# Kernel tuning notes

Measured on AMD Instinct MI355X. Metric: run time of the kernel, lower is better.

Reference implementation:

```python
import jax, jax.numpy as jnp
import numpy as np

N = 8192
F_IN = 256
F_OUT = 64
ALPHA = 0.2  # LeakyReLU negative slope
EDGE_P = 0.004  # ~33 avg degree


def setup_inputs() -> dict:
    key = jax.random.key(0)
    k1, k2, k3, k4 = jax.random.split(key, 4)
    h = jax.random.normal(k1, (N, F_IN), dtype=jnp.float32)
    # xavier-ish scale for params
    W = jax.random.normal(k2, (F_IN, F_OUT), dtype=jnp.float32) * np.float32(np.sqrt(2.0 / (F_IN + F_OUT)))
    a = jax.random.normal(k3, (2 * F_OUT, 1), dtype=jnp.float32) * np.float32(np.sqrt(2.0 / (2 * F_OUT + 1)))
    adj = (jax.random.uniform(k4, (N, N)) < EDGE_P).astype(jnp.float32)
    return {"h": h, "adj": adj, "W": W, "a": a}


def reference(h, adj, W, a):
    f_out = W.shape[1]
    Wh = h @ W  # [N, F_OUT]
    # NOTE: original uses a[out_features:] for the source (row) term
    wh1 = Wh @ a[f_out:, :]  # [N, 1]
    wh2 = Wh @ a[:f_out, :]  # [N, 1]
    # e[u, i] = wh1[u] + wh2[i] only where adj nonzero; zero elsewhere (NO -inf mask,
    # faithful to the original: softmax sees zeros at non-edges)
    e = jnp.where(adj != 0, wh1 + wh2.T, jnp.float32(0.0))  # [N, N]
    e = jnp.where(e >= 0, e, ALPHA * e)  # LeakyReLU
    attention = jax.nn.softmax(e, axis=1)  # [N, N]
    # dropout p=0.0 -> identity
    h_prime = attention @ Wh  # [N, F_OUT]
    return jax.nn.elu(h_prime)  # concat=True
```

## Files before the change

### kernel.cpp

```cpp
#include <hip/hip_runtime.h>
#include <hip/hip_bf16.h>
#include <math.h>

#define N     8192
#define F_IN  256
#define F_OUT 64
#define ALPHA 0.2f

__global__ __launch_bounds__(256) void gat_wh_kernel(
    const float* __restrict__ h,
    const float* __restrict__ W,
    const float* __restrict__ a,
    float* __restrict__ Wh,
    float* __restrict__ wh1,
    float* __restrict__ wh2,
    float* __restrict__ colpart)
{
    __shared__ float s_h[4][F_IN];
    __shared__ float s_cp[256];

    const int tid = threadIdx.x;
    const int wv  = tid >> 6;
    const int ln  = tid & 63;
    const int u   = blockIdx.x * 4 + wv;

    const float4* hrow = (const float4*)(h + (size_t)u * F_IN);
    ((float4*)s_h[wv])[ln] = hrow[ln];
    __syncthreads();

    float acc = 0.f;
    const float4* sh4 = (const float4*)s_h[wv];
#pragma unroll 8
    for (int k4 = 0; k4 < F_IN / 4; ++k4) {
        float4 hv = sh4[k4];
        int k = k4 * 4;
        acc += hv.x * W[(k + 0) * F_OUT + ln];
        acc += hv.y * W[(k + 1) * F_OUT + ln];
        acc += hv.z * W[(k + 2) * F_OUT + ln];
        acc += hv.w * W[(k + 3) * F_OUT + ln];
    }

    Wh[(size_t)u * F_OUT + ln] = acc;

    float p1 = acc * a[F_OUT + ln];
    float p2 = acc * a[ln];
#pragma unroll
    for (int off = 32; off > 0; off >>= 1) {
        p1 += __shfl_down(p1, off);
        p2 += __shfl_down(p2, off);
    }
    if (ln == 0) {
        wh1[u] = p1;
        wh2[u] = p2;
    }

    s_cp[tid] = acc;
    __syncthreads();
    if (tid < 64) {
        colpart[(size_t)blockIdx.x * 64 + tid] =
            s_cp[tid] + s_cp[tid + 64] + s_cp[tid + 128] + s_cp[tid + 192];
    }
}

__global__ __launch_bounds__(256) void gat_colsum_kernel(
    const float* __restrict__ colpart,
    float* __restrict__ colsum)
{
    __shared__ float r[256];
    const int f = blockIdx.x;
    const int tid = threadIdx.x;
    float s = 0.f;
    for (int b = tid; b < 2048; b += 256) s += colpart[(size_t)b * 64 + f];
    r[tid] = s;
    __syncthreads();
    if (tid < 128) r[tid] += r[tid + 128];
    __syncthreads();
    if (tid < 64) {
        float x = r[tid] + r[tid + 64];
#pragma unroll
        for (int off = 32; off > 0; off >>= 1) x += __shfl_down(x, off);
        if (tid == 0) colsum[f] = x;
    }
}

#define CHUNK  2048
#define PASSES (N / CHUNK)

__global__ __launch_bounds__(256) void gat_main_kernel(
    const float* __restrict__ adj,
    const float* __restrict__ Wh,
    const float* __restrict__ wh1,
    const float* __restrict__ wh2,
    const float* __restrict__ colsum,
    float* __restrict__ out)
{
    __shared__ int   s_idx[CHUNK];
    __shared__ float s_w[CHUNK];
    __shared__ float s_red[256];
    __shared__ int   s_cnt;

    const int tid = threadIdx.x;
    const int u   = blockIdx.x;
    const int f   = tid & 63;
    const int g   = tid >> 6;

    const float wh1u = wh1[u];
    const float* __restrict__ arow = adj + (size_t)u * N;

    float acc  = 0.f;
    float sumw = 0.f;

    for (int p = 0; p < PASSES; ++p) {
        if (tid == 0) s_cnt = 0;
        __syncthreads();

        const int base = p * CHUNK + tid * 8;
        float4 v0 = *(const float4*)(arow + base);
        float4 v1 = *(const float4*)(arow + base + 4);
        float vals[8] = {v0.x, v0.y, v0.z, v0.w, v1.x, v1.y, v1.z, v1.w};
#pragma unroll
        for (int j = 0; j < 8; ++j) {
            if (vals[j] != 0.f) {
                int col = base + j;
                float e = wh1u + wh2[col];
                e = (e >= 0.f) ? e : ALPHA * e;
                float w = expm1f(e);
                sumw += w;
                int pos = atomicAdd(&s_cnt, 1);
                s_idx[pos] = col;
                s_w[pos]   = w;
            }
        }
        __syncthreads();
        const int nE = s_cnt;
        __syncthreads();

        for (int e = g; e < nE; e += 4) {
            acc += s_w[e] * Wh[(size_t)s_idx[e] * F_OUT + f];
        }
    }

    s_red[tid] = sumw;
    __syncthreads();
    if (tid < 128) s_red[tid] += s_red[tid + 128];
    __syncthreads();
    if (tid < 64) {
        float x = s_red[tid] + s_red[tid + 64];
#pragma unroll
        for (int off = 32; off > 0; off >>= 1) x += __shfl_down(x, off);
        if (tid == 0) s_red[0] = x;
    }
    __syncthreads();
    const float denom = s_red[0] + (float)N;
    __syncthreads();

    s_red[tid] = acc;
    __syncthreads();
    if (tid < 64) {
        float tot = s_red[tid] + s_red[tid + 64] + s_red[tid + 128] + s_red[tid + 192];
        float val = (tot + colsum[tid]) / denom;
        out[(size_t)u * F_OUT + tid] = (val > 0.f) ? val : expm1f(val);
    }
}

extern "C" void kernel_launch(void* const* d_in, const int* in_sizes, int n_in,
                              void* d_out, int out_size, void* d_ws, size_t ws_size,
                              hipStream_t stream) {
    const float* h   = (const float*)d_in[0];
    const float* adj = (const float*)d_in[1];
    const float* W   = (const float*)d_in[2];
    const float* a   = (const float*)d_in[3];
    float* out = (float*)d_out;

    float* ws      = (float*)d_ws;
    float* Wh      = ws;
    float* wh1     = Wh + (size_t)N * F_OUT;
    float* wh2     = wh1 + N;
    float* colpart = wh2 + N;
    float* colsum  = colpart + 2048 * 64;

    gat_wh_kernel<<<N / 4, 256, 0, stream>>>(h, W, a, Wh, wh1, wh2, colpart);
    gat_colsum_kernel<<<64, 256, 0, stream>>>(colpart, colsum);
    gat_main_kernel<<<N, 256, 0, stream>>>(adj, Wh, wh1, wh2, colsum, out);
}
```

Baseline: 393.5 us.

## Assign one wavefront per row and compact edges with ballot instead of shared atomics

The main kernel now gives each 64-lane wavefront one adjacency row, four rows per block, in place of one 256-thread block per row. Each wavefront scans the row with vector loads, finds nonzero edges with a ballot mask, and all lanes walk that mask together to accumulate the weighted Wh features. This removes the shared-memory atomic compaction, the block barriers and the cross-wave reductions. In exchange, each wave handles all edges of its row serially, and the adj loads have a different coalescing pattern.

```diff
diff --git a/kernel.cpp b/kernel.cpp
--- a/kernel.cpp
+++ b/kernel.cpp
@@ -83,9 +83,6 @@
     }
 }
 
-#define CHUNK  2048
-#define PASSES (N / CHUNK)
-
 __global__ __launch_bounds__(256) void gat_main_kernel(
     const float* __restrict__ adj,
     const float* __restrict__ Wh,
@@ -94,15 +91,10 @@
     const float* __restrict__ colsum,
     float* __restrict__ out)
 {
-    __shared__ int   s_idx[CHUNK];
-    __shared__ float s_w[CHUNK];
-    __shared__ float s_red[256];
-    __shared__ int   s_cnt;
-
-    const int tid = threadIdx.x;
-    const int u   = blockIdx.x;
-    const int f   = tid & 63;
-    const int g   = tid >> 6;
+    const int tid  = threadIdx.x;
+    const int lane = tid & 63;
+    const int wv   = tid >> 6;
+    const int u    = blockIdx.x * 4 + wv;
 
     const float wh1u = wh1[u];
     const float* __restrict__ arow = adj + (size_t)u * N;
@@ -110,57 +102,30 @@
     float acc  = 0.f;
     float sumw = 0.f;
 
-    for (int p = 0; p < PASSES; ++p) {
-        if (tid == 0) s_cnt = 0;
-        __syncthreads();
-
-        const int base = p * CHUNK + tid * 8;
-        float4 v0 = *(const float4*)(arow + base);
-        float4 v1 = *(const float4*)(arow + base + 4);
+    for (int it = 0; it < 16; ++it) {
+        const int cbase = it * 512;
+        const float4* p = (const float4*)(arow + cbase + lane * 8);
+        float4 v0 = p[0];
+        float4 v1 = p[1];
         float vals[8] = {v0.x, v0.y, v0.z, v0.w, v1.x, v1.y, v1.z, v1.w};
 #pragma unroll
         for (int j = 0; j < 8; ++j) {
-            if (vals[j] != 0.f) {
-                int col = base + j;
+            unsigned long long m = __ballot(vals[j] != 0.f);
+            while (m) {
+                int l = __ffsll((long long)m) - 1;
+                m &= m - 1;
+                int col = cbase + l * 8 + j;
                 float e = wh1u + wh2[col];
                 e = (e >= 0.f) ? e : ALPHA * e;
                 float w = expm1f(e);
                 sumw += w;
-                int pos = atomicAdd(&s_cnt, 1);
-                s_idx[pos] = col;
-                s_w[pos]   = w;
+                acc += w * Wh[(size_t)col * F_OUT + lane];
             }
-        }
-        __syncthreads();
-        const int nE = s_cnt;
-        __syncthreads();
-
-        for (int e = g; e < nE; e += 4) {
-            acc += s_w[e] * Wh[(size_t)s_idx[e] * F_OUT + f];
         }
     }
 
-    s_red[tid] = sumw;
-    __syncthreads();
-    if (tid < 128) s_red[tid] += s_red[tid + 128];
-    __syncthreads();
-    if (tid < 64) {
-        float x = s_red[tid] + s_red[tid + 64];
-#pragma unroll
-        for (int off = 32; off > 0; off >>= 1) x += __shfl_down(x, off);
-        if (tid == 0) s_red[0] = x;
-    }
-    __syncthreads();
-    const float denom = s_red[0] + (float)N;
-    __syncthreads();
-
-    s_red[tid] = acc;
-    __syncthreads();
-    if (tid < 64) {
-        float tot = s_red[tid] + s_red[tid + 64] + s_red[tid + 128] + s_red[tid + 192];
-        float val = (tot + colsum[tid]) / denom;
-        out[(size_t)u * F_OUT + tid] = (val > 0.f) ? val : expm1f(val);
-    }
+    float val = (acc + colsum[lane]) / (sumw + (float)N);
+    out[(size_t)u * F_OUT + lane] = (val > 0.f) ? val : expm1f(val);
 }
 
 extern "C" void kernel_launch(void* const* d_in, const int* in_sizes, int n_in,
@@ -181,5 +146,5 @@
 
     gat_wh_kernel<<<N / 4, 256, 0, stream>>>(h, W, a, Wh, wh1, wh2, colpart);
     gat_colsum_kernel<<<64, 256, 0, stream>>>(colpart, colsum);
-    gat_main_kernel<<<N, 256, 0, stream>>>(adj, Wh, wh1, wh2, colsum, out);
+    gat_main_kernel<<<N / 4, 256, 0, stream>>>(adj, Wh, wh1, wh2, colsum, out);
 }
```

Measured after the change: 395.2 us. About the same (+0.4%).
